# Kernel optimization log

Hardware: AMD Instinct MI355X
Metric: run time of the kernel (lower is better)

## Reference

```python
import jax, jax.numpy as jnp
import numpy as np

B, L, D = 2048, 200, 128
HID = [80, 40]


def setup_inputs() -> dict:
    key = jax.random.key(0)
    ks = jax.random.split(key, 10)
    hist_emb = jax.random.normal(ks[0], (B, L, D), dtype=jnp.float32)
    target_emb = jax.random.normal(ks[1], (B, D), dtype=jnp.float32)
    mask = jax.random.randint(ks[2], (B, L), 0, 2, dtype=jnp.int32)
    # MLP params: (4D -> 80 -> 40 -> 1), Kaiming-uniform-ish like nn.Linear default
    dims = [4 * D] + HID + [1]
    params = {}
    for i in range(len(dims) - 1):
        fan_in = dims[i]
        bound = 1.0 / np.sqrt(fan_in)
        params[f"W{i}"] = jax.random.uniform(ks[3 + 2 * i], (dims[i], dims[i + 1]), minval=-bound, maxval=bound, dtype=jnp.float32)
        params[f"b{i}"] = jax.random.uniform(ks[4 + 2 * i], (dims[i + 1],), minval=-bound, maxval=bound, dtype=jnp.float32)
    return {"hist_emb": hist_emb, "target_emb": target_emb, "mask": mask, **params}


def reference(hist_emb, target_emb, mask, W0, b0, W1, b1, W2, b2):
    # hist_emb: (B,L,D); target_emb: (B,D); mask: (B,L)
    target = target_emb[:, None, :]                       # (B,1,D) -> broadcast over L
    diff = hist_emb - target
    prod = hist_emb * target
    tgt = jnp.broadcast_to(target, hist_emb.shape)
    feat = jnp.concatenate([hist_emb, tgt, diff, prod], axis=-1)  # (B,L,4D)
    h = jax.nn.relu(jnp.einsum("blf,fh->blh", feat, W0) + b0)
    h = jax.nn.relu(jnp.einsum("blf,fh->blh", h, W1) + b1)
    scores = (jnp.einsum("blf,fh->blh", h, W2) + b2)[..., 0]      # (B,L)
    m = mask.astype(scores.dtype)
    logits = scores + (1.0 - m) * -1e9
    attn = jax.nn.softmax(logits, axis=1)                 # (B,L)
    user_interest = jnp.einsum("bl,bld->bd", attn, hist_emb)
    return user_interest, attn
```

## Files before the change

### kernel.cpp

```cpp
#include <hip/hip_runtime.h>
#include <hip/hip_bf16.h>

#define B_  2048
#define L_  200
#define D_  128
#define H0_ 80
#define H1_ 40

typedef __attribute__((ext_vector_type(8))) short short8;
typedef __attribute__((ext_vector_type(4))) float floatx4;

__device__ __forceinline__ short f2bf(float f) {
    unsigned u = __float_as_uint(f);
    u += 0x7fffu + ((u >> 16) & 1u);
    return (short)(u >> 16);
}

__global__ __launch_bounds__(256, 3) void din_kernel(
    const float* __restrict__ hist,
    const float* __restrict__ tgt,
    const int*   __restrict__ mask,
    const float* __restrict__ W0,
    const float* __restrict__ b0,
    const float* __restrict__ W1,
    const float* __restrict__ b1,
    const float* __restrict__ W2,
    const float* __restrict__ b2,
    float* __restrict__ out)
{
    __shared__ __align__(16) short w0t[H0_][136];
    __shared__ __align__(16) short w1t[48][104];
    __shared__ __align__(16) short h0t[4][16][104];
    __shared__ float tgs[D_];
    __shared__ float beffp[2][H0_];
    __shared__ float beffs[H0_];
    __shared__ float b1w2[2][48];
    __shared__ float scores[208];
    __shared__ float attns[L_];
    __shared__ float partial[2][D_];
    __shared__ float red[8];

    const int tid = threadIdx.x;
    const int b   = blockIdx.x;
    float* ui_out   = out + (size_t)b * D_;
    float* attn_out = out + (size_t)B_ * D_ + (size_t)b * L_;

    if (tid < D_) tgs[tid] = tgt[(size_t)b * D_ + tid];
    if (tid < 48) {
        b1w2[0][tid] = (tid < H1_) ? b1[tid] : 0.f;
        b1w2[1][tid] = (tid < H1_) ? W2[tid] : 0.f;
    }
    for (int i = tid; i < 48 * 104; i += 256) {
        int n = i / 104, k = i - n * 104;
        w1t[n][k] = (n < H1_ && k < H0_) ? f2bf(W1[k * H1_ + n]) : (short)0;
    }
    for (int i = tid; i < 4 * 16 * 104 / 2; i += 256) ((int*)h0t)[i] = 0;
    __syncthreads();

    for (int i = tid; i < D_ * H0_; i += 256) {
        int d = i / H0_, h = i - d * H0_;
        float v = W0[i] + W0[256 * H0_ + i] + tgs[d] * W0[384 * H0_ + i];
        w0t[h][d] = f2bf(v);
    }
    if (tid < 160) {
        int h = tid % H0_, c = tid / H0_;
        float s = 0.f;
        #pragma unroll 4
        for (int d = c * 64; d < c * 64 + 64; ++d)
            s += tgs[d] * (W0[(128 + d) * H0_ + h] - W0[(256 + d) * H0_ + h]);
        beffp[c][h] = s;
    }
    __syncthreads();
    if (tid < H0_) beffs[tid] = b0[tid] + beffp[0][tid] + beffp[1][tid];
    __syncthreads();

    const int wave = tid >> 6, lane = tid & 63;
    const int col = lane & 15, quad = lane >> 4;
    const float b2v = b2[0];

    for (int mt = wave; mt < 13; mt += 4) {
        const int m0 = mt * 16;
        int mrow = m0 + col; if (mrow > L_ - 1) mrow = L_ - 1;
        const float* ap = hist + ((size_t)b * L_ + mrow) * D_ + quad * 8;

        short8 afrag[4];
        #pragma unroll
        for (int ks = 0; ks < 4; ++ks) {
            floatx4 x = *(const floatx4*)(ap + ks * 32);
            floatx4 y = *(const floatx4*)(ap + ks * 32 + 4);
            short8 a;
            a[0] = f2bf(x[0]); a[1] = f2bf(x[1]); a[2] = f2bf(x[2]); a[3] = f2bf(x[3]);
            a[4] = f2bf(y[0]); a[5] = f2bf(y[1]); a[6] = f2bf(y[2]); a[7] = f2bf(y[3]);
            afrag[ks] = a;
        }

        floatx4 c0[5];
        #pragma unroll
        for (int nt = 0; nt < 5; ++nt) c0[nt] = (floatx4)0.f;
        #pragma unroll
        for (int ks = 0; ks < 4; ++ks) {
            #pragma unroll
            for (int nt = 0; nt < 5; ++nt) {
                short8 bf = *(const short8*)&w0t[nt * 16 + col][ks * 32 + quad * 8];
                c0[nt] = __builtin_amdgcn_mfma_f32_16x16x32_bf16(afrag[ks], bf, c0[nt], 0, 0, 0);
            }
        }
        #pragma unroll
        for (int nt = 0; nt < 5; ++nt) {
            #pragma unroll
            for (int r = 0; r < 4; ++r) {
                float v = c0[nt][r] + beffs[nt * 16 + col];
                v = v > 0.f ? v : 0.f;
                h0t[wave][quad * 4 + r][nt * 16 + col] = f2bf(v);
            }
        }

        floatx4 c1[3];
        #pragma unroll
        for (int nt = 0; nt < 3; ++nt) c1[nt] = (floatx4)0.f;
        #pragma unroll
        for (int ks = 0; ks < 3; ++ks) {
            short8 a1 = *(const short8*)&h0t[wave][col][ks * 32 + quad * 8];
            #pragma unroll
            for (int nt = 0; nt < 3; ++nt) {
                short8 bf = *(const short8*)&w1t[nt * 16 + col][ks * 32 + quad * 8];
                c1[nt] = __builtin_amdgcn_mfma_f32_16x16x32_bf16(a1, bf, c1[nt], 0, 0, 0);
            }
        }
        float s4[4] = {0.f, 0.f, 0.f, 0.f};
        #pragma unroll
        for (int nt = 0; nt < 3; ++nt) {
            float bb = b1w2[0][nt * 16 + col];
            float ww = b1w2[1][nt * 16 + col];
            #pragma unroll
            for (int r = 0; r < 4; ++r) {
                float v = c1[nt][r] + bb;
                v = v > 0.f ? v : 0.f;
                s4[r] += v * ww;
            }
        }
        #pragma unroll
        for (int r = 0; r < 4; ++r) {
            s4[r] += __shfl_xor(s4[r], 1, 16);
            s4[r] += __shfl_xor(s4[r], 2, 16);
            s4[r] += __shfl_xor(s4[r], 4, 16);
            s4[r] += __shfl_xor(s4[r], 8, 16);
        }
        if (col == 0) {
            #pragma unroll
            for (int r = 0; r < 4; ++r)
                scores[m0 + quad * 4 + r] = s4[r] + b2v;
        }
    }
    __syncthreads();

    float sc;
    if (tid < L_) {
        sc = scores[tid];
        if (mask[(size_t)b * L_ + tid] == 0) sc -= 1e9f;
    } else {
        sc = -3.0e38f;
    }
    float m = sc;
    #pragma unroll
    for (int off = 32; off >= 1; off >>= 1) m = fmaxf(m, __shfl_xor(m, off, 64));
    int wid = tid >> 6;
    if ((tid & 63) == 0) red[wid] = m;
    __syncthreads();
    m = fmaxf(fmaxf(red[0], red[1]), fmaxf(red[2], red[3]));
    float e = (tid < L_) ? __expf(sc - m) : 0.f;
    float s = e;
    #pragma unroll
    for (int off = 32; off >= 1; off >>= 1) s += __shfl_xor(s, off, 64);
    if ((tid & 63) == 0) red[4 + wid] = s;
    __syncthreads();
    s = red[4] + red[5] + red[6] + red[7];
    float inv = 1.0f / s;
    if (tid < L_) {
        float av = e * inv;
        attns[tid] = av;
        attn_out[tid] = av;
    }
    __syncthreads();

    {
        const int half = tid >> 7, d = tid & 127;
        const float* hb = hist + ((size_t)b * L_ + half * 100) * D_ + d;
        float acc = 0.f;
        #pragma unroll 10
        for (int l = 0; l < 100; ++l)
            acc = fmaf(attns[half * 100 + l], hb[(size_t)l * D_], acc);
        partial[half][d] = acc;
    }
    __syncthreads();
    if (tid < D_) ui_out[tid] = partial[0][tid] + partial[1][tid];
}

extern "C" void kernel_launch(void* const* d_in, const int* in_sizes, int n_in,
                              void* d_out, int out_size, void* d_ws, size_t ws_size,
                              hipStream_t stream) {
    const float* hist = (const float*)d_in[0];
    const float* tgt  = (const float*)d_in[1];
    const int*   mask = (const int*)d_in[2];
    const float* W0   = (const float*)d_in[3];
    const float* b0   = (const float*)d_in[4];
    const float* W1   = (const float*)d_in[5];
    const float* b1   = (const float*)d_in[6];
    const float* W2   = (const float*)d_in[7];
    const float* b2   = (const float*)d_in[8];
    din_kernel<<<B_, 256, 0, stream>>>(hist, tgt, mask, W0, b0, W1, b1, W2, b2,
                                       (float*)d_out);
}
```

Baseline: 400.5 us.

## Split per-batch weight folding into a prep kernel and stream bf16 weights from workspace

Moves the per-sample folding of W0 with the target embedding, the effective bias and the W1 transpose into a separate prep kernel that writes bf16 weights to workspace. The main kernel then reads B fragments straight from global memory instead of building them in LDS, which cuts its prologue and shared memory so occupancy can be raised to 4 blocks. The cost is an extra launch and about 40 MB of workspace traffic written and reread, plus uncached global B-fragment loads inside the MFMA loop. The mask load is also hoisted to kernel start.

```diff
diff --git a/kernel.cpp b/kernel.cpp
--- a/kernel.cpp
+++ b/kernel.cpp
@@ -15,24 +15,69 @@
     u += 0x7fffu + ((u >> 16) & 1u);
     return (short)(u >> 16);
 }
-
-__global__ __launch_bounds__(256, 3) void din_kernel(
-    const float* __restrict__ hist,
-    const float* __restrict__ tgt,
-    const int*   __restrict__ mask,
-    const float* __restrict__ W0,
-    const float* __restrict__ b0,
-    const float* __restrict__ W1,
-    const float* __restrict__ b1,
-    const float* __restrict__ W2,
+__device__ __forceinline__ float bf2f(short s) {
+    return __uint_as_float(((unsigned)(unsigned short)s) << 16);
+}
+
+#define W1T_SOFF  (B_ * H0_ * D_)
+#define BEFF_FOFF ((B_ * H0_ * D_ + 48 * 96) / 2)
+
+__global__ __launch_bounds__(256, 2) void prep_kernel(
+    const float* __restrict__ tgt, const float* __restrict__ W0,
+    const float* __restrict__ b0, const float* __restrict__ W1,
+    short* __restrict__ w0t, short* __restrict__ w1t, float* __restrict__ beff)
+{
+    __shared__ float w0s[H0_][130];
+    __shared__ short w0d[H0_][130];
+    __shared__ float tgs[D_];
+    __shared__ float red2[2][H0_];
+
+    const int tid = threadIdx.x;
+    for (int i = tid; i < D_ * H0_; i += 256) {
+        int d = i / H0_, h = i - d * H0_;
+        w0s[h][d] = W0[i] + W0[256 * H0_ + i];
+        w0d[h][d] = f2bf(W0[384 * H0_ + i]);
+    }
+    if (blockIdx.x == 0) {
+        for (int i = tid; i < 48 * 96; i += 256) {
+            int n = i / 96, k = i - n * 96;
+            w1t[i] = (n < H1_ && k < H0_) ? f2bf(W1[k * H1_ + n]) : (short)0;
+        }
+    }
+    for (int bb = 0; bb < 4; ++bb) {
+        const int b = blockIdx.x * 4 + bb;
+        __syncthreads();
+        if (tid < D_) tgs[tid] = tgt[(size_t)b * D_ + tid];
+        __syncthreads();
+        short* outp = w0t + (size_t)b * H0_ * D_;
+        for (int i = tid; i < H0_ * D_; i += 256) {
+            int h = i >> 7, d = i & 127;
+            outp[i] = f2bf(w0s[h][d] + tgs[d] * bf2f(w0d[h][d]));
+        }
+        if (tid < 160) {
+            int seg = tid / H0_, h = tid - seg * H0_;
+            float s = 0.f;
+            #pragma unroll 8
+            for (int dd = 0; dd < 64; ++dd) {
+                int d = seg * 64 + dd;
+                s += tgs[d] * (W0[(128 + d) * H0_ + h] - W0[(256 + d) * H0_ + h]);
+            }
+            red2[seg][h] = s;
+        }
+        __syncthreads();
+        if (tid < H0_)
+            beff[(size_t)b * H0_ + tid] = b0[tid] + red2[0][tid] + red2[1][tid];
+    }
+}
+
+__global__ __launch_bounds__(256, 4) void din_main(
+    const float* __restrict__ hist, const int* __restrict__ mask,
+    const float* __restrict__ b1, const float* __restrict__ W2,
     const float* __restrict__ b2,
-    float* __restrict__ out)
+    const short* __restrict__ w0t, const short* __restrict__ w1t,
+    const float* __restrict__ beff, float* __restrict__ out)
 {
-    __shared__ __align__(16) short w0t[H0_][136];
-    __shared__ __align__(16) short w1t[48][104];
     __shared__ __align__(16) short h0t[4][16][104];
-    __shared__ float tgs[D_];
-    __shared__ float beffp[2][H0_];
     __shared__ float beffs[H0_];
     __shared__ float b1w2[2][48];
     __shared__ float scores[208];
@@ -45,38 +90,21 @@
     float* ui_out   = out + (size_t)b * D_;
     float* attn_out = out + (size_t)B_ * D_ + (size_t)b * L_;
 
-    if (tid < D_) tgs[tid] = tgt[(size_t)b * D_ + tid];
+    const float b2v = b2[0];
+    int mv = 1;
+    if (tid < L_) mv = mask[(size_t)b * L_ + tid];
+
+    if (tid < H0_) beffs[tid] = beff[(size_t)b * H0_ + tid];
     if (tid < 48) {
         b1w2[0][tid] = (tid < H1_) ? b1[tid] : 0.f;
         b1w2[1][tid] = (tid < H1_) ? W2[tid] : 0.f;
     }
-    for (int i = tid; i < 48 * 104; i += 256) {
-        int n = i / 104, k = i - n * 104;
-        w1t[n][k] = (n < H1_ && k < H0_) ? f2bf(W1[k * H1_ + n]) : (short)0;
-    }
     for (int i = tid; i < 4 * 16 * 104 / 2; i += 256) ((int*)h0t)[i] = 0;
-    __syncthreads();
-
-    for (int i = tid; i < D_ * H0_; i += 256) {
-        int d = i / H0_, h = i - d * H0_;
-        float v = W0[i] + W0[256 * H0_ + i] + tgs[d] * W0[384 * H0_ + i];
-        w0t[h][d] = f2bf(v);
-    }
-    if (tid < 160) {
-        int h = tid % H0_, c = tid / H0_;
-        float s = 0.f;
-        #pragma unroll 4
-        for (int d = c * 64; d < c * 64 + 64; ++d)
-            s += tgs[d] * (W0[(128 + d) * H0_ + h] - W0[(256 + d) * H0_ + h]);
-        beffp[c][h] = s;
-    }
-    __syncthreads();
-    if (tid < H0_) beffs[tid] = b0[tid] + beffp[0][tid] + beffp[1][tid];
     __syncthreads();
 
     const int wave = tid >> 6, lane = tid & 63;
     const int col = lane & 15, quad = lane >> 4;
-    const float b2v = b2[0];
+    const short* w0b = w0t + (size_t)b * H0_ * D_;
 
     for (int mt = wave; mt < 13; mt += 4) {
         const int m0 = mt * 16;
@@ -97,12 +125,13 @@
         floatx4 c0[5];
         #pragma unroll
         for (int nt = 0; nt < 5; ++nt) c0[nt] = (floatx4)0.f;
+        const short* bp = w0b + col * D_ + quad * 8;
         #pragma unroll
         for (int ks = 0; ks < 4; ++ks) {
             #pragma unroll
             for (int nt = 0; nt < 5; ++nt) {
-                short8 bf = *(const short8*)&w0t[nt * 16 + col][ks * 32 + quad * 8];
-                c0[nt] = __builtin_amdgcn_mfma_f32_16x16x32_bf16(afrag[ks], bf, c0[nt], 0, 0, 0);
+                short8 bfr = *(const short8*)(bp + nt * 16 * D_ + ks * 32);
+                c0[nt] = __builtin_amdgcn_mfma_f32_16x16x32_bf16(afrag[ks], bfr, c0[nt], 0, 0, 0);
             }
         }
         #pragma unroll
@@ -118,13 +147,14 @@
         floatx4 c1[3];
         #pragma unroll
         for (int nt = 0; nt < 3; ++nt) c1[nt] = (floatx4)0.f;
+        const short* wp = w1t + col * 96 + quad * 8;
         #pragma unroll
         for (int ks = 0; ks < 3; ++ks) {
             short8 a1 = *(const short8*)&h0t[wave][col][ks * 32 + quad * 8];
             #pragma unroll
             for (int nt = 0; nt < 3; ++nt) {
-                short8 bf = *(const short8*)&w1t[nt * 16 + col][ks * 32 + quad * 8];
-                c1[nt] = __builtin_amdgcn_mfma_f32_16x16x32_bf16(a1, bf, c1[nt], 0, 0, 0);
+                short8 bfr = *(const short8*)(wp + nt * 16 * 96 + ks * 32);
+                c1[nt] = __builtin_amdgcn_mfma_f32_16x16x32_bf16(a1, bfr, c1[nt], 0, 0, 0);
             }
         }
         float s4[4] = {0.f, 0.f, 0.f, 0.f};
@@ -157,7 +187,7 @@
     float sc;
     if (tid < L_) {
         sc = scores[tid];
-        if (mask[(size_t)b * L_ + tid] == 0) sc -= 1e9f;
+        if (mv == 0) sc -= 1e9f;
     } else {
         sc = -3.0e38f;
     }
@@ -208,6 +238,12 @@
     const float* b1   = (const float*)d_in[6];
     const float* W2   = (const float*)d_in[7];
     const float* b2   = (const float*)d_in[8];
-    din_kernel<<<B_, 256, 0, stream>>>(hist, tgt, mask, W0, b0, W1, b1, W2, b2,
-                                       (float*)d_out);
-}
+
+    short* w0t = (short*)d_ws;
+    short* w1t = (short*)d_ws + W1T_SOFF;
+    float* beff = (float*)d_ws + BEFF_FOFF;
+
+    prep_kernel<<<512, 256, 0, stream>>>(tgt, W0, b0, W1, w0t, w1t, beff);
+    din_main<<<B_, 256, 0, stream>>>(hist, mask, b1, W2, b2, w0t, w1t, beff,
+                                     (float*)d_out);
+}
```

Result: slower. 444.0 us (+10.9%).
